# Kernel tuning notes

Hardware: AMD Instinct MI355X
Metric: run time of the kernel (lower is better)

Reference implementation:

```python
import jax, jax.numpy as jnp
import numpy as np

B, S, D = 2, 2048, 1024
H, KH, HD = 16, 4, 64          # n_heads, n_kv_heads, head_dim
REP = H // KH                  # GQA repeat factor
ROPE_THETA = 10000.0


def _rope(x, cos, sin):
    """x: [B,S,nh,HD]; cos/sin: [S,HD//2]. Interleaved-pair complex rotation."""
    xr = x.reshape(*x.shape[:-1], HD // 2, 2)
    x0, x1 = xr[..., 0], xr[..., 1]
    c = cos[None, :, None, :]  # [1,S,1,HD//2]
    s = sin[None, :, None, :]
    o0 = x0 * c - x1 * s
    o1 = x0 * s + x1 * c
    return jnp.stack([o0, o1], axis=-1).reshape(x.shape)


def setup_inputs() -> dict:
    key = jax.random.key(0)
    ks = jax.random.split(key, 5)
    x = jax.random.normal(ks[0], (B, S, D), dtype=jnp.float32)
    sc = 0.02
    wq = jax.random.normal(ks[1], (D, H * HD), dtype=jnp.float32) * sc
    wk = jax.random.normal(ks[2], (D, KH * HD), dtype=jnp.float32) * sc
    wv = jax.random.normal(ks[3], (D, KH * HD), dtype=jnp.float32) * sc
    wo = jax.random.normal(ks[4], (H * HD, D), dtype=jnp.float32) * sc
    # RoPE tables (precomputed buffers in the torch model)
    inv_freq = 1.0 / (ROPE_THETA ** (np.arange(0, HD, 2, dtype=np.float32) / HD))
    ang = np.arange(S, dtype=np.float32)[:, None] * inv_freq[None, :]  # [S,HD//2]
    freqs_cos = jnp.asarray(np.cos(ang))
    freqs_sin = jnp.asarray(np.sin(ang))
    # additive causal mask [1,1,S,S]
    neg = jnp.finfo(jnp.float32).min
    mask = jnp.where(jnp.tril(jnp.ones((S, S), dtype=bool)), 0.0, neg)[None, None]
    return {"x": x, "wq": wq, "wk": wk, "wv": wv, "wo": wo,
            "freqs_cos": freqs_cos, "freqs_sin": freqs_sin, "mask": mask}


def reference(x, wq, wk, wv, wo, freqs_cos, freqs_sin, mask):
    scale = 1.0 / jnp.sqrt(jnp.float32(HD))
    q = (x @ wq).reshape(B, S, H, HD)
    k = (x @ wk).reshape(B, S, KH, HD)
    v = (x @ wv).reshape(B, S, KH, HD)
    q = _rope(q, freqs_cos, freqs_sin)
    k = _rope(k, freqs_cos, freqs_sin)
    # GQA: query head h uses kv head h // REP == grouping consecutive q heads
    q = q.reshape(B, S, KH, REP, HD).transpose(0, 2, 3, 1, 4)  # [B,KH,REP,S,HD]
    k = k.transpose(0, 2, 1, 3)                                # [B,KH,S,HD]
    v = v.transpose(0, 2, 1, 3)
    scores = jnp.einsum('bkrqd,bksd->bkrqs', q, k) * scale     # [B,KH,REP,S,S]
    scores = scores + mask[:, :, None]                         # broadcast over REP
    attn = jax.nn.softmax(scores, axis=-1)
    out = jnp.einsum('bkrqs,bksd->bkrqd', attn, v)             # [B,KH,REP,S,HD]
    out = out.transpose(0, 3, 1, 2, 4).reshape(B, S, H * HD)
    return out @ wo
```

## Files before the change

kernel.cpp:

```cpp
#include <hip/hip_runtime.h>
#include <hip/hip_bf16.h>

using bf16 = __hip_bfloat16;
typedef short bf16x8 __attribute__((ext_vector_type(8)));
typedef float f32x4 __attribute__((ext_vector_type(4)));

#define CB 2
#define CS 2048
#define CD 1024
#define CH 16
#define CKH 4
#define CHD 64
#define CREP 4
#define CNQ (CH*CHD)
#define CNKV (CKH*CHD)
#define CM (CB*CS)

__device__ __forceinline__ unsigned short f2bf(float f) {
  union { float f; unsigned int i; } c; c.f = f;
  unsigned int r = c.i + 0x7FFFu + ((c.i >> 16) & 1u);
  return (unsigned short)(r >> 16);
}
__device__ __forceinline__ float bf2f(unsigned short u) {
  union { unsigned int i; float f; } c;
  c.i = ((unsigned int)u) << 16;
  return c.f;
}
__device__ __forceinline__ void gload_lds16(const void* g, void* l) {
  __builtin_amdgcn_global_load_lds(
      (const __attribute__((address_space(1))) void*)g,
      (__attribute__((address_space(3))) void*)l, 16, 0, 0);
}

__global__ __launch_bounds__(256) void gemm_mfma_kernel(
    const bf16* __restrict__ A, const bf16* __restrict__ Bt,
    float* __restrict__ C, int Mm, int Nn, int Kk, int lda)
{
  __shared__ __align__(16) bf16 As[2][64 * 32];
  __shared__ __align__(16) bf16 Bs[2][128 * 32];
  const int tid = threadIdx.x;
  const int lane = tid & 63;
  const int l15 = lane & 15;
  const int g = lane >> 4;
  const int wid = tid >> 6;
  const int wr = (wid >> 1) * 32;
  const int wc = (wid & 1) * 64;
  const int m0 = blockIdx.x * 64;
  const int n0 = blockIdx.y * 128;

  f32x4 acc[2][4];
  #pragma unroll
  for (int i = 0; i < 2; ++i)
    #pragma unroll
    for (int j = 0; j < 4; ++j)
      acc[i][j] = (f32x4){0.f, 0.f, 0.f, 0.f};

  const int sr = tid >> 2;
  const int sc = (tid & 3) * 8;
  const bf16* aSrc = A + (size_t)(m0 + sr) * lda + sc;
  const bf16* bSrc = Bt + (size_t)(n0 + sr) * Kk + sc;
  const int sOff = (tid & 192) * 8;

#define GSTAGE(bi, k0) do {                                             \
    gload_lds16(aSrc + (k0),                     &As[bi][sOff]);        \
    gload_lds16(bSrc + (k0),                     &Bs[bi][sOff]);        \
    gload_lds16(bSrc + 64 * (size_t)Kk + (k0),   &Bs[bi][sOff + 2048]); \
  } while (0)

  const int nt = Kk >> 5;
  int bi = 0;
  GSTAGE(0, 0);
  for (int t = 0; t < nt; ++t) {
    if (t + 1 < nt) {
      GSTAGE(bi ^ 1, (t + 1) * 32);
      asm volatile("s_waitcnt vmcnt(3)" ::: "memory");
    } else {
      asm volatile("s_waitcnt vmcnt(0)" ::: "memory");
    }
    __builtin_amdgcn_s_barrier();
    asm volatile("" ::: "memory");

    bf16x8 af[2], bfr[4];
    #pragma unroll
    for (int mt = 0; mt < 2; ++mt)
      af[mt] = *(const bf16x8*)&As[bi][(wr + mt * 16 + l15) * 32 + g * 8];
    #pragma unroll
    for (int nt2 = 0; nt2 < 4; ++nt2)
      bfr[nt2] = *(const bf16x8*)&Bs[bi][(wc + nt2 * 16 + l15) * 32 + g * 8];
    #pragma unroll
    for (int mt = 0; mt < 2; ++mt)
      #pragma unroll
      for (int nt2 = 0; nt2 < 4; ++nt2)
        acc[mt][nt2] = __builtin_amdgcn_mfma_f32_16x16x32_bf16(af[mt], bfr[nt2], acc[mt][nt2], 0, 0, 0);

    asm volatile("" ::: "memory");
    __builtin_amdgcn_s_barrier();
    bi ^= 1;
  }
#undef GSTAGE

  #pragma unroll
  for (int mt = 0; mt < 2; ++mt)
    #pragma unroll
    for (int r4 = 0; r4 < 4; ++r4) {
      const size_t row = (size_t)(m0 + wr + mt * 16 + 4 * g + r4);
      #pragma unroll
      for (int nt2 = 0; nt2 < 4; ++nt2)
        C[row * Nn + n0 + wc + nt2 * 16 + l15] = acc[mt][nt2][r4];
    }
}

__global__ __launch_bounds__(256) void gemm_qkv_rope_kernel(
    const bf16* __restrict__ A, const bf16* __restrict__ Bt,
    const float* __restrict__ fc, const float* __restrict__ fs,
    bf16* __restrict__ qb, bf16* __restrict__ kb, bf16* __restrict__ vt)
{
  __shared__ __align__(16) bf16 As[2][64 * 32];
  __shared__ __align__(16) bf16 Bs[2][128 * 32];
  const int tid = threadIdx.x;
  const int lane = tid & 63;
  const int l15 = lane & 15;
  const int g = lane >> 4;
  const int wid = tid >> 6;
  const int wr = (wid >> 1) * 32;
  const int wc = (wid & 1) * 64;
  const int m0 = blockIdx.x * 64;
  const int n0 = blockIdx.y * 128;
  const int Kk = CD;

  f32x4 acc[2][4];
  #pragma unroll
  for (int i = 0; i < 2; ++i)
    #pragma unroll
    for (int j = 0; j < 4; ++j)
      acc[i][j] = (f32x4){0.f, 0.f, 0.f, 0.f};

  const int sr = tid >> 2;
  const int sc = (tid & 3) * 8;
  const bf16* aSrc = A + (size_t)(m0 + sr) * Kk + sc;
  const bf16* bSrc = Bt + (size_t)(n0 + sr) * Kk + sc;
  const int sOff = (tid & 192) * 8;

#define GSTAGE(bi, k0) do {                                             \
    gload_lds16(aSrc + (k0),                     &As[bi][sOff]);        \
    gload_lds16(bSrc + (k0),                     &Bs[bi][sOff]);        \
    gload_lds16(bSrc + 64 * (size_t)Kk + (k0),   &Bs[bi][sOff + 2048]); \
  } while (0)

  const int nt = Kk >> 5;
  int bi = 0;
  GSTAGE(0, 0);
  for (int t = 0; t < nt; ++t) {
    if (t + 1 < nt) {
      GSTAGE(bi ^ 1, (t + 1) * 32);
      asm volatile("s_waitcnt vmcnt(3)" ::: "memory");
    } else {
      asm volatile("s_waitcnt vmcnt(0)" ::: "memory");
    }
    __builtin_amdgcn_s_barrier();
    asm volatile("" ::: "memory");

    bf16x8 af[2], bfr[4];
    #pragma unroll
    for (int mt = 0; mt < 2; ++mt)
      af[mt] = *(const bf16x8*)&As[bi][(wr + mt * 16 + l15) * 32 + g * 8];
    #pragma unroll
    for (int nt2 = 0; nt2 < 4; ++nt2)
      bfr[nt2] = *(const bf16x8*)&Bs[bi][(wc + nt2 * 16 + l15) * 32 + g * 8];
    #pragma unroll
    for (int mt = 0; mt < 2; ++mt)
      #pragma unroll
      for (int nt2 = 0; nt2 < 4; ++nt2)
        acc[mt][nt2] = __builtin_amdgcn_mfma_f32_16x16x32_bf16(af[mt], bfr[nt2], acc[mt][nt2], 0, 0, 0);

    asm volatile("" ::: "memory");
    __builtin_amdgcn_s_barrier();
    bi ^= 1;
  }
#undef GSTAGE

  if (blockIdx.y < 10) {
    const bool isq = (blockIdx.y < 8);
    const float qsc = isq ? 0.18033688f : 1.0f;
    #pragma unroll
    for (int mt = 0; mt < 2; ++mt)
      #pragma unroll
      for (int r4 = 0; r4 < 4; ++r4) {
        int m = m0 + wr + mt * 16 + 4 * g + r4;
        int s = m & (CS - 1), bb = m >> 11;
        #pragma unroll
        for (int nt2 = 0; nt2 < 4; ++nt2) {
          int n = n0 + wc + nt2 * 16 + l15;
          int d = n & 63;
          float val = acc[mt][nt2][r4];
          float par = __shfl_xor(val, 1, 64);
          float cv = fc[s * 32 + (d >> 1)];
          float sv = fs[s * 32 + (d >> 1)];
          float o = (d & 1) ? (par * sv + val * cv) : (val * cv - par * sv);
          o *= qsc;
          if (isq) {
            int h = n >> 6;
            ((unsigned short*)qb)[(((size_t)bb * CH + h) * CS + s) * CHD + d] = f2bf(o);
          } else {
            int kh = (n >> 6) - 16;
            ((unsigned short*)kb)[(((size_t)bb * CKH + kh) * CS + s) * CHD + d] = f2bf(o);
          }
        }
      }
  } else {
    #pragma unroll
    for (int mt = 0; mt < 2; ++mt) {
      int mb = m0 + wr + mt * 16 + 4 * g;
      int s0 = mb & (CS - 1), bb = mb >> 11;
      #pragma unroll
      for (int nt2 = 0; nt2 < 4; ++nt2) {
        int n = n0 + wc + nt2 * 16 + l15;
        int d = n & 63;
        int kh = (n >> 6) - 20;
        ushort4 pk = make_ushort4(f2bf(acc[mt][nt2][0]), f2bf(acc[mt][nt2][1]),
                                  f2bf(acc[mt][nt2][2]), f2bf(acc[mt][nt2][3]));
        *(ushort4*)&((unsigned short*)vt)[(((size_t)bb * CKH + kh) * CHD + d) * CS + s0] = pk;
      }
    }
  }
}

__global__ __launch_bounds__(256) void prep_kernel(
    const float* __restrict__ x, bf16* __restrict__ xb,
    const float* __restrict__ wq, const float* __restrict__ wk,
    const float* __restrict__ wv, const float* __restrict__ wo,
    bf16* __restrict__ wqkvt, bf16* __restrict__ wot)
{
  const int tid = threadIdx.x;
  int bid = blockIdx.x;
  if (bid < 2048) {
    int i = (bid * 256 + tid) * 8;
    float4 a = *(const float4*)&x[i];
    float4 b = *(const float4*)&x[i + 4];
    unsigned short* o = (unsigned short*)xb + i;
    *(ushort4*)o = make_ushort4(f2bf(a.x), f2bf(a.y), f2bf(a.z), f2bf(a.w));
    *(ushort4*)(o + 4) = make_ushort4(f2bf(b.x), f2bf(b.y), f2bf(b.z), f2bf(b.w));
    return;
  }
  bid -= 2048;
  const float* W; bf16* Wt; int Nn, bx, by;
  if (bid < 256)      { W = wq; Wt = wqkvt;                      Nn = 1024; bx = bid & 15;        by = bid >> 4; }
  else if (bid < 320) { W = wk; Wt = wqkvt + (size_t)1024 * CD;  Nn = 256;  bx = (bid-256) & 15;  by = (bid-256) >> 4; }
  else if (bid < 384) { W = wv; Wt = wqkvt + (size_t)1280 * CD;  Nn = 256;  bx = (bid-320) & 15;  by = (bid-320) >> 4; }
  else                { W = wo; Wt = wot;                        Nn = 1024; bx = (bid-384) & 15;  by = (bid-384) >> 4; }
  const int Kk = 1024;
  const int k0 = bx * 64;
  const int n0 = by * 64;

  __shared__ float T[64][65];
  const int lr = tid >> 4;
  const int lc = (tid & 15) * 4;
  #pragma unroll
  for (int i = 0; i < 4; ++i) {
    float4 v = *(const float4*)&W[(size_t)(k0 + lr + i * 16) * Nn + n0 + lc];
    T[lr + i * 16][lc + 0] = v.x;
    T[lr + i * 16][lc + 1] = v.y;
    T[lr + i * 16][lc + 2] = v.z;
    T[lr + i * 16][lc + 3] = v.w;
  }
  __syncthreads();
  const int rn = tid >> 3;
  const int ck = (tid & 7) * 8;
  #pragma unroll
  for (int i = 0; i < 2; ++i) {
    int nn = rn + i * 32;
    unsigned short u[8];
    #pragma unroll
    for (int e = 0; e < 8; ++e) u[e] = f2bf(T[ck + e][nn]);
    unsigned short* dst = (unsigned short*)Wt + (size_t)(n0 + nn) * Kk + k0 + ck;
    *(ushort4*)dst = make_ushort4(u[0], u[1], u[2], u[3]);
    *(ushort4*)(dst + 4) = make_ushort4(u[4], u[5], u[6], u[7]);
  }
}

__global__ __launch_bounds__(256, 2) void flash_split_kernel(
    const bf16* __restrict__ qb, const bf16* __restrict__ kb,
    const bf16* __restrict__ vt, bf16* __restrict__ oc0,
    bf16* __restrict__ ob, float2* __restrict__ ml)
{
  __shared__ __align__(16) char arena[51200];
  char* KL = arena;
  char* VL = arena + 16384;
  const int tid = threadIdx.x;
  const int lane = tid & 63;
  const int wid = tid >> 6;
  unsigned short* PLW = (unsigned short*)(arena + 32768) + wid * 2304;
  const int l15 = lane & 15;
  const int g = lane >> 4;
  const int blk = blockIdx.x;
  const int chunk = blk & 1;
  const int grp = (blk >> 1) & 7;
  const int idx = blk >> 4;
  const int qt = 63 - idx;
  const int kh = grp & 3;
  const int b = grp >> 2;
  const int h = kh * CREP + wid;
  const int N64 = (qt >> 1) + 1;
  const int hc = N64 >> 1;
  const int tbeg = chunk ? hc : 0;
  const int tend = chunk ? N64 : hc;

  const bf16* qbase = qb + ((size_t)(b * CH + h) * CS + qt * 32) * CHD;
  const bf16* kbase = kb + (size_t)(b * CKH + kh) * CS * CHD;
  const bf16* vbase = vt + (size_t)(b * CKH + kh) * CHD * CS;

  bf16x8 qf[2][2];
  #pragma unroll
  for (int qs = 0; qs < 2; ++qs)
    #pragma unroll
    for (int c = 0; c < 2; ++c)
      qf[qs][c] = *(const bf16x8*)(qbase + (qs * 16 + l15) * CHD + c * 32 + g * 8);

  bf16x8 ones;
  #pragma unroll
  for (int e = 0; e < 8; ++e) ones[e] = (short)0x3F80;

  f32x4 oacc[2][4];
  f32x4 lacc[2];
  #pragma unroll
  for (int qs = 0; qs < 2; ++qs) {
    lacc[qs] = (f32x4){0.f, 0.f, 0.f, 0.f};
    #pragma unroll
    for (int dt = 0; dt < 4; ++dt)
      oacc[qs][dt] = (f32x4){0.f, 0.f, 0.f, 0.f};
  }
  float mrow[2] = {-1e30f, -1e30f};

  const int slr = tid >> 3;
  const int scg = (tid & 7) ^ (slr & 7);
  const bf16* kstage = kbase + (size_t)slr * CHD + scg * 8;
  const bf16* vstage = vbase + (size_t)slr * CS + scg * 8;
  char* kdst = KL + wid * 1024;
  char* vdst = VL + wid * 1024;

#define STAGE(bi, t64) do {                                        \
    const bf16* ks_ = kstage + (size_t)(t64) * 64 * CHD;           \
    const bf16* vs_ = vstage + (t64) * 64;                         \
    gload_lds16(ks_,            kdst + (bi) * 8192);               \
    gload_lds16(ks_ + 32 * CHD, kdst + (bi) * 8192 + 4096);        \
    gload_lds16(vs_,            vdst + (bi) * 8192);               \
    gload_lds16(vs_ + 32 * CS,  vdst + (bi) * 8192 + 4096);        \
  } while (0)

  if (tbeg < tend) {
    int bi = 0;
    STAGE(0, tbeg);
    for (int t = tbeg; t < tend; ++t) {
      if (t + 1 < tend) {
        STAGE(bi ^ 1, t + 1);
        asm volatile("s_waitcnt vmcnt(4)" ::: "memory");
      } else {
        asm volatile("s_waitcnt vmcnt(0)" ::: "memory");
      }
      __builtin_amdgcn_s_barrier();
      asm volatile("" ::: "memory");

      const char* KB = KL + bi * 8192;
      const char* VB = VL + bi * 8192;
      bf16x8 kfr[4][2], vfr[4][2];
      #pragma unroll
      for (int kt = 0; kt < 4; ++kt) {
        int row = kt * 16 + l15;
        #pragma unroll
        for (int c = 0; c < 2; ++c)
          kfr[kt][c] = *(const bf16x8*)(KB + row * 128 + (((c * 4 + g) ^ (row & 7)) << 4));
      }
      #pragma unroll
      for (int dt = 0; dt < 4; ++dt) {
        int row = dt * 16 + l15;
        #pragma unroll
        for (int st = 0; st < 2; ++st)
          vfr[dt][st] = *(const bf16x8*)(VB + row * 128 + (((st * 4 + g) ^ (row & 7)) << 4));
      }

      f32x4 sacc[4][2];
      #pragma unroll
      for (int kt = 0; kt < 4; ++kt)
        #pragma unroll
        for (int qs = 0; qs < 2; ++qs)
          sacc[kt][qs] = (f32x4){0.f, 0.f, 0.f, 0.f};
      #pragma unroll
      for (int c = 0; c < 2; ++c)
        #pragma unroll
        for (int kt = 0; kt < 4; ++kt)
          #pragma unroll
          for (int qs = 0; qs < 2; ++qs)
            sacc[kt][qs] = __builtin_amdgcn_mfma_f32_16x16x32_bf16(kfr[kt][c], qf[qs][c], sacc[kt][qs], 0, 0, 0);

      const bool diag = (t == N64 - 1);
      #pragma unroll
      for (int qs = 0; qs < 2; ++qs) {
        float pe[16];
        float pm = -1e30f;
        #pragma unroll
        for (int kt = 0; kt < 4; ++kt)
          #pragma unroll
          for (int r = 0; r < 4; ++r) {
            float v = sacc[kt][qs][r];
            if (diag) {
              int koff = t * 64 + kt * 16 + 4 * g + r;
              if (koff > qt * 32 + qs * 16 + l15) v = -1e30f;
            }
            pe[kt * 4 + r] = v;
            pm = fmaxf(pm, v);
          }
        if (__any(pm > mrow[qs] + 8.0f)) {
          pm = fmaxf(pm, __shfl_xor(pm, 16, 64));
          pm = fmaxf(pm, __shfl_xor(pm, 32, 64));
          float nm = fmaxf(mrow[qs], pm);
          float corr = exp2f(mrow[qs] - nm);
          mrow[qs] = nm;
          lacc[qs] *= corr;
          #pragma unroll
          for (int dt = 0; dt < 4; ++dt) oacc[qs][dt] *= corr;
        }
        #pragma unroll
        for (int i = 0; i < 16; ++i)
          pe[i] = exp2f(pe[i] - mrow[qs]);
        #pragma unroll
        for (int kt = 0; kt < 4; ++kt) {
          unsigned int lo = (__float_as_uint(pe[kt * 4 + 1]) & 0xFFFF0000u) |
                            (__float_as_uint(pe[kt * 4 + 0]) >> 16);
          unsigned int hi = (__float_as_uint(pe[kt * 4 + 3]) & 0xFFFF0000u) |
                            (__float_as_uint(pe[kt * 4 + 2]) >> 16);
          *(uint2*)&PLW[(qs * 16 + l15) * 72 + kt * 16 + 4 * g] = make_uint2(lo, hi);
        }
      }

      #pragma unroll
      for (int qs = 0; qs < 2; ++qs) {
        #pragma unroll
        for (int st = 0; st < 2; ++st) {
          bf16x8 pf = *(const bf16x8*)&PLW[(qs * 16 + l15) * 72 + st * 32 + g * 8];
          lacc[qs] = __builtin_amdgcn_mfma_f32_16x16x32_bf16(ones, pf, lacc[qs], 0, 0, 0);
          #pragma unroll
          for (int dt = 0; dt < 4; ++dt)
            oacc[qs][dt] = __builtin_amdgcn_mfma_f32_16x16x32_bf16(vfr[dt][st], pf, oacc[qs][dt], 0, 0, 0);
        }
      }

      asm volatile("" ::: "memory");
      __builtin_amdgcn_s_barrier();
      bi ^= 1;
    }
  }
#undef STAGE

  unsigned short* pdst = (unsigned short*)(chunk ? ob : oc0);
  #pragma unroll
  for (int qs = 0; qs < 2; ++qs) {
    int qg = qt * 32 + qs * 16 + l15;
    unsigned short* prow = pdst + (size_t)(b * CS + qg) * CNQ + h * CHD;
    #pragma unroll
    for (int dt = 0; dt < 4; ++dt)
      *(ushort4*)&prow[dt * 16 + 4 * g] =
          make_ushort4(f2bf(oacc[qs][dt][0]), f2bf(oacc[qs][dt][1]),
                       f2bf(oacc[qs][dt][2]), f2bf(oacc[qs][dt][3]));
    if (g == 0)
      ml[(((size_t)chunk * CB + b) * CH + h) * CS + qg] = make_float2(mrow[qs], lacc[qs][0]);
  }
}

__global__ __launch_bounds__(256) void merge_kernel(
    const bf16* __restrict__ oc0, bf16* __restrict__ ob,
    const float2* __restrict__ ml)
{
  const int e8 = blockIdx.x * 256 + threadIdx.x;
  const size_t off = (size_t)e8 * 8;
  const int row = (int)(off >> 10);
  const int col = (int)(off & 1023);
  const int h = col >> 6;
  const int b = row >> 11;
  const int s = row & (CS - 1);
  float2 ml0 = ml[(((size_t)0 * CB + b) * CH + h) * CS + s];
  float2 ml1 = ml[(((size_t)1 * CB + b) * CH + h) * CS + s];
  float M = fmaxf(ml0.x, ml1.x);
  float c0 = exp2f(ml0.x - M), c1 = exp2f(ml1.x - M);
  float inv = 1.0f / (c0 * ml0.y + c1 * ml1.y);
  ushort4 a0 = *(const ushort4*)((const unsigned short*)oc0 + off);
  ushort4 a1 = *(const ushort4*)((const unsigned short*)oc0 + off + 4);
  ushort4 b0 = *(const ushort4*)((const unsigned short*)ob + off);
  ushort4 b1 = *(const ushort4*)((const unsigned short*)ob + off + 4);
  unsigned short r[8];
  const unsigned short* p0 = &a0.x;
  const unsigned short* p1 = &b0.x;
  #pragma unroll
  for (int i = 0; i < 4; ++i)
    r[i] = f2bf((c0 * bf2f(p0[i]) + c1 * bf2f(p1[i])) * inv);
  p0 = &a1.x; p1 = &b1.x;
  #pragma unroll
  for (int i = 0; i < 4; ++i)
    r[4 + i] = f2bf((c0 * bf2f(p0[i]) + c1 * bf2f(p1[i])) * inv);
  *(ushort4*)((unsigned short*)ob + off) = make_ushort4(r[0], r[1], r[2], r[3]);
  *(ushort4*)((unsigned short*)ob + off + 4) = make_ushort4(r[4], r[5], r[6], r[7]);
}

extern "C" void kernel_launch(void* const* d_in, const int* in_sizes, int n_in,
                              void* d_out, int out_size, void* d_ws, size_t ws_size,
                              hipStream_t stream)
{
  const float* x  = (const float*)d_in[0];
  const float* wq = (const float*)d_in[1];
  const float* wk = (const float*)d_in[2];
  const float* wv = (const float*)d_in[3];
  const float* wo = (const float*)d_in[4];
  const float* fc = (const float*)d_in[5];
  const float* fs = (const float*)d_in[6];
  float* out = (float*)d_out;

  char* ws = (char*)d_ws;
  bf16*   x_b   = (bf16*)(ws);
  bf16*   wqkvt = (bf16*)(ws + 8388608);
  bf16*   wot   = (bf16*)(ws + 11534336);
  bf16*   q_b   = (bf16*)(ws + 13631488);
  bf16*   k_b   = (bf16*)(ws + 22020096);
  bf16*   v_t   = (bf16*)(ws + 24117248);
  bf16*   o_b   = (bf16*)(ws);
  bf16*   oc0   = (bf16*)(ws + 26214400);
  float2* mlb   = (float2*)(ws + 34603008);

  prep_kernel<<<2688, 256, 0, stream>>>(x, x_b, wq, wk, wv, wo, wqkvt, wot);
  gemm_qkv_rope_kernel<<<dim3(64, 12), 256, 0, stream>>>(x_b, wqkvt, fc, fs, q_b, k_b, v_t);
  flash_split_kernel<<<1024, 256, 0, stream>>>(q_b, k_b, v_t, oc0, o_b, mlb);
  merge_kernel<<<2048, 256, 0, stream>>>(oc0, o_b, mlb);
  gemm_mfma_kernel<<<dim3(64, 8), 256, 0, stream>>>(o_b, wot, out, CM, CD, CNQ, CNQ);
}
```

Before: 115.4 us.

## Widen GEMM K-tile to 64 with XOR-swizzled LDS and prioritize attention MFMA

Both projection GEMM kernels now stage 64-wide K slices instead of 32, using an XOR-swizzled LDS layout that mirrors the attention kernel's, and issue two MFMAs per fragment pair each iteration. This halves the number of barrier-separated iterations and aims to reduce LDS bank conflicts on fragment reads. The cost is double the LDS footprint per block, which may lower occupancy. The attention kernel also raises wave priority around its MFMA sections with s_setprio, to favour issuing matrix work over other waves' softmax.

```diff
diff --git a/kernel.cpp b/kernel.cpp
--- a/kernel.cpp
+++ b/kernel.cpp
@@ -36,8 +36,8 @@
     const bf16* __restrict__ A, const bf16* __restrict__ Bt,
     float* __restrict__ C, int Mm, int Nn, int Kk, int lda)
 {
-  __shared__ __align__(16) bf16 As[2][64 * 32];
-  __shared__ __align__(16) bf16 Bs[2][128 * 32];
+  __shared__ __align__(16) bf16 As[2][64 * 64];
+  __shared__ __align__(16) bf16 Bs[2][128 * 64];
   const int tid = threadIdx.x;
   const int lane = tid & 63;
   const int l15 = lane & 15;
@@ -55,43 +55,59 @@
     for (int j = 0; j < 4; ++j)
       acc[i][j] = (f32x4){0.f, 0.f, 0.f, 0.f};
 
-  const int sr = tid >> 2;
-  const int sc = (tid & 3) * 8;
-  const bf16* aSrc = A + (size_t)(m0 + sr) * lda + sc;
-  const bf16* bSrc = Bt + (size_t)(n0 + sr) * Kk + sc;
-  const int sOff = (tid & 192) * 8;
-
-#define GSTAGE(bi, k0) do {                                             \
-    gload_lds16(aSrc + (k0),                     &As[bi][sOff]);        \
-    gload_lds16(bSrc + (k0),                     &Bs[bi][sOff]);        \
-    gload_lds16(bSrc + 64 * (size_t)Kk + (k0),   &Bs[bi][sOff + 2048]); \
+  const int slr = tid >> 3;
+  const int scg = (tid & 7) ^ (slr & 7);
+  const bf16* aStage = A + (size_t)(m0 + slr) * lda + scg * 8;
+  const bf16* bStage = Bt + (size_t)(n0 + slr) * Kk + scg * 8;
+  char* aDst = (char*)As + wid * 1024;
+  char* bDst = (char*)Bs + wid * 1024;
+
+#define GSTAGE(bi, k0) do {                                                   \
+    gload_lds16(aStage + (k0),                      aDst + (bi) * 8192);      \
+    gload_lds16(aStage + 32 * (size_t)lda + (k0),   aDst + (bi) * 8192 + 4096); \
+    gload_lds16(bStage + (k0),                      bDst + (bi) * 16384);     \
+    gload_lds16(bStage + 32 * (size_t)Kk + (k0),    bDst + (bi) * 16384 + 4096); \
+    gload_lds16(bStage + 64 * (size_t)Kk + (k0),    bDst + (bi) * 16384 + 8192); \
+    gload_lds16(bStage + 96 * (size_t)Kk + (k0),    bDst + (bi) * 16384 + 12288); \
   } while (0)
 
-  const int nt = Kk >> 5;
+  const int nt = Kk >> 6;
   int bi = 0;
   GSTAGE(0, 0);
   for (int t = 0; t < nt; ++t) {
     if (t + 1 < nt) {
-      GSTAGE(bi ^ 1, (t + 1) * 32);
-      asm volatile("s_waitcnt vmcnt(3)" ::: "memory");
+      GSTAGE(bi ^ 1, (t + 1) * 64);
+      asm volatile("s_waitcnt vmcnt(6)" ::: "memory");
     } else {
       asm volatile("s_waitcnt vmcnt(0)" ::: "memory");
     }
     __builtin_amdgcn_s_barrier();
     asm volatile("" ::: "memory");
 
-    bf16x8 af[2], bfr[4];
-    #pragma unroll
-    for (int mt = 0; mt < 2; ++mt)
-      af[mt] = *(const bf16x8*)&As[bi][(wr + mt * 16 + l15) * 32 + g * 8];
-    #pragma unroll
-    for (int nt2 = 0; nt2 < 4; ++nt2)
-      bfr[nt2] = *(const bf16x8*)&Bs[bi][(wc + nt2 * 16 + l15) * 32 + g * 8];
-    #pragma unroll
-    for (int mt = 0; mt < 2; ++mt)
-      #pragma unroll
-      for (int nt2 = 0; nt2 < 4; ++nt2)
-        acc[mt][nt2] = __builtin_amdgcn_mfma_f32_16x16x32_bf16(af[mt], bfr[nt2], acc[mt][nt2], 0, 0, 0);
+    const char* AB = (const char*)As + bi * 8192;
+    const char* BB = (const char*)Bs + bi * 16384;
+    bf16x8 af[2][2], bfr[4][2];
+    #pragma unroll
+    for (int mt = 0; mt < 2; ++mt) {
+      int row = wr + mt * 16 + l15;
+      #pragma unroll
+      for (int c = 0; c < 2; ++c)
+        af[mt][c] = *(const bf16x8*)(AB + row * 128 + (((c * 4 + g) ^ (row & 7)) << 4));
+    }
+    #pragma unroll
+    for (int nt2 = 0; nt2 < 4; ++nt2) {
+      int row = wc + nt2 * 16 + l15;
+      #pragma unroll
+      for (int c = 0; c < 2; ++c)
+        bfr[nt2][c] = *(const bf16x8*)(BB + row * 128 + (((c * 4 + g) ^ (row & 7)) << 4));
+    }
+    #pragma unroll
+    for (int c = 0; c < 2; ++c)
+      #pragma unroll
+      for (int mt = 0; mt < 2; ++mt)
+        #pragma unroll
+        for (int nt2 = 0; nt2 < 4; ++nt2)
+          acc[mt][nt2] = __builtin_amdgcn_mfma_f32_16x16x32_bf16(af[mt][c], bfr[nt2][c], acc[mt][nt2], 0, 0, 0);
 
     asm volatile("" ::: "memory");
     __builtin_amdgcn_s_barrier();
@@ -115,8 +131,8 @@
     const float* __restrict__ fc, const float* __restrict__ fs,
     bf16* __restrict__ qb, bf16* __restrict__ kb, bf16* __restrict__ vt)
 {
-  __shared__ __align__(16) bf16 As[2][64 * 32];
-  __shared__ __align__(16) bf16 Bs[2][128 * 32];
+  __shared__ __align__(16) bf16 As[2][64 * 64];
+  __shared__ __align__(16) bf16 Bs[2][128 * 64];
   const int tid = threadIdx.x;
   const int lane = tid & 63;
   const int l15 = lane & 15;
@@ -135,43 +151,59 @@
     for (int j = 0; j < 4; ++j)
       acc[i][j] = (f32x4){0.f, 0.f, 0.f, 0.f};
 
-  const int sr = tid >> 2;
-  const int sc = (tid & 3) * 8;
-  const bf16* aSrc = A + (size_t)(m0 + sr) * Kk + sc;
-  const bf16* bSrc = Bt + (size_t)(n0 + sr) * Kk + sc;
-  const int sOff = (tid & 192) * 8;
-
-#define GSTAGE(bi, k0) do {                                             \
-    gload_lds16(aSrc + (k0),                     &As[bi][sOff]);        \
-    gload_lds16(bSrc + (k0),                     &Bs[bi][sOff]);        \
-    gload_lds16(bSrc + 64 * (size_t)Kk + (k0),   &Bs[bi][sOff + 2048]); \
+  const int slr = tid >> 3;
+  const int scg = (tid & 7) ^ (slr & 7);
+  const bf16* aStage = A + (size_t)(m0 + slr) * Kk + scg * 8;
+  const bf16* bStage = Bt + (size_t)(n0 + slr) * Kk + scg * 8;
+  char* aDst = (char*)As + wid * 1024;
+  char* bDst = (char*)Bs + wid * 1024;
+
+#define GSTAGE(bi, k0) do {                                                   \
+    gload_lds16(aStage + (k0),                      aDst + (bi) * 8192);      \
+    gload_lds16(aStage + 32 * (size_t)Kk + (k0),    aDst + (bi) * 8192 + 4096); \
+    gload_lds16(bStage + (k0),                      bDst + (bi) * 16384);     \
+    gload_lds16(bStage + 32 * (size_t)Kk + (k0),    bDst + (bi) * 16384 + 4096); \
+    gload_lds16(bStage + 64 * (size_t)Kk + (k0),    bDst + (bi) * 16384 + 8192); \
+    gload_lds16(bStage + 96 * (size_t)Kk + (k0),    bDst + (bi) * 16384 + 12288); \
   } while (0)
 
-  const int nt = Kk >> 5;
+  const int nt = Kk >> 6;
   int bi = 0;
   GSTAGE(0, 0);
   for (int t = 0; t < nt; ++t) {
     if (t + 1 < nt) {
-      GSTAGE(bi ^ 1, (t + 1) * 32);
-      asm volatile("s_waitcnt vmcnt(3)" ::: "memory");
+      GSTAGE(bi ^ 1, (t + 1) * 64);
+      asm volatile("s_waitcnt vmcnt(6)" ::: "memory");
     } else {
       asm volatile("s_waitcnt vmcnt(0)" ::: "memory");
     }
     __builtin_amdgcn_s_barrier();
     asm volatile("" ::: "memory");
 
-    bf16x8 af[2], bfr[4];
-    #pragma unroll
-    for (int mt = 0; mt < 2; ++mt)
-      af[mt] = *(const bf16x8*)&As[bi][(wr + mt * 16 + l15) * 32 + g * 8];
-    #pragma unroll
-    for (int nt2 = 0; nt2 < 4; ++nt2)
-      bfr[nt2] = *(const bf16x8*)&Bs[bi][(wc + nt2 * 16 + l15) * 32 + g * 8];
-    #pragma unroll
-    for (int mt = 0; mt < 2; ++mt)
-      #pragma unroll
-      for (int nt2 = 0; nt2 < 4; ++nt2)
-        acc[mt][nt2] = __builtin_amdgcn_mfma_f32_16x16x32_bf16(af[mt], bfr[nt2], acc[mt][nt2], 0, 0, 0);
+    const char* AB = (const char*)As + bi * 8192;
+    const char* BB = (const char*)Bs + bi * 16384;
+    bf16x8 af[2][2], bfr[4][2];
+    #pragma unroll
+    for (int mt = 0; mt < 2; ++mt) {
+      int row = wr + mt * 16 + l15;
+      #pragma unroll
+      for (int c = 0; c < 2; ++c)
+        af[mt][c] = *(const bf16x8*)(AB + row * 128 + (((c * 4 + g) ^ (row & 7)) << 4));
+    }
+    #pragma unroll
+    for (int nt2 = 0; nt2 < 4; ++nt2) {
+      int row = wc + nt2 * 16 + l15;
+      #pragma unroll
+      for (int c = 0; c < 2; ++c)
+        bfr[nt2][c] = *(const bf16x8*)(BB + row * 128 + (((c * 4 + g) ^ (row & 7)) << 4));
+    }
+    #pragma unroll
+    for (int c = 0; c < 2; ++c)
+      #pragma unroll
+      for (int mt = 0; mt < 2; ++mt)
+        #pragma unroll
+        for (int nt2 = 0; nt2 < 4; ++nt2)
+          acc[mt][nt2] = __builtin_amdgcn_mfma_f32_16x16x32_bf16(af[mt][c], bfr[nt2][c], acc[mt][nt2], 0, 0, 0);
 
     asm volatile("" ::: "memory");
     __builtin_amdgcn_s_barrier();
@@ -384,6 +416,7 @@
         #pragma unroll
         for (int qs = 0; qs < 2; ++qs)
           sacc[kt][qs] = (f32x4){0.f, 0.f, 0.f, 0.f};
+      __builtin_amdgcn_s_setprio(1);
       #pragma unroll
       for (int c = 0; c < 2; ++c)
         #pragma unroll
@@ -391,6 +424,7 @@
           #pragma unroll
           for (int qs = 0; qs < 2; ++qs)
             sacc[kt][qs] = __builtin_amdgcn_mfma_f32_16x16x32_bf16(kfr[kt][c], qf[qs][c], sacc[kt][qs], 0, 0, 0);
+      __builtin_amdgcn_s_setprio(0);
 
       const bool diag = (t == N64 - 1);
       #pragma unroll
@@ -432,6 +466,7 @@
         }
       }
 
+      __builtin_amdgcn_s_setprio(1);
       #pragma unroll
       for (int qs = 0; qs < 2; ++qs) {
         #pragma unroll
@@ -443,6 +478,7 @@
             oacc[qs][dt] = __builtin_amdgcn_mfma_f32_16x16x32_bf16(vfr[dt][st], pf, oacc[qs][dt], 0, 0, 0);
         }
       }
+      __builtin_amdgcn_s_setprio(0);
 
       asm volatile("" ::: "memory");
       __builtin_amdgcn_s_barrier();
```

Result: faster. 106.0 us (-8.1%).
